# Optimization experiments

Measured on AMD Instinct MI355X. Metric: run time of the kernel, lower is better.

Reference implementation:

```python
import jax, jax.numpy as jnp
import numpy as np

HIDDEN = 512
STATE_DIM = 256
H = 8
D = STATE_DIM // H  # 32
B = 8
T = 4096


def setup_inputs() -> dict:
    key = jax.random.key(0)
    ks = jax.random.split(key, 12)
    s = 0.02
    return {
        "hidden_states": jax.random.normal(ks[0], (B, T, HIDDEN), jnp.float32),
        "state": jnp.zeros((B, H, D, D), jnp.float32),
        "W_k": jax.random.normal(ks[1], (STATE_DIM, HIDDEN), jnp.float32) * s,
        "W_v": jax.random.normal(ks[2], (STATE_DIM, HIDDEN), jnp.float32) * s,
        "W_q": jax.random.normal(ks[3], (STATE_DIM, HIDDEN), jnp.float32) * s,
        "W_beta": jax.random.normal(ks[4], (STATE_DIM, HIDDEN), jnp.float32) * s,
        "b_beta": jnp.zeros((STATE_DIM,), jnp.float32),
        "W_alpha": jax.random.normal(ks[5], (STATE_DIM, HIDDEN), jnp.float32) * s,
        "b_alpha": jnp.full((STATE_DIM,), 2.0, jnp.float32),
        "W_out": jax.random.normal(ks[6], (HIDDEN, STATE_DIM), jnp.float32) * s,
        "gate_W": jax.random.normal(ks[7], (STATE_DIM, HIDDEN), jnp.float32) * s,
        "norm_w": jnp.ones((STATE_DIM,), jnp.float32),
    }


def _rms_norm(x, w, eps=1e-6):
    dtype = x.dtype
    xf = x.astype(jnp.float32)
    n = xf * jax.lax.rsqrt(jnp.mean(xf * xf, axis=-1, keepdims=True) + eps)
    return (n * w).astype(dtype)


def reference(hidden_states, state, W_k, W_v, W_q, W_beta, b_beta, W_alpha, b_alpha, W_out, gate_W, norm_w):
    bsz, seq_len, _ = hidden_states.shape
    # projections -> (B, T, H, D)
    k = (hidden_states @ W_k.T).reshape(bsz, seq_len, H, D)
    v = (hidden_states @ W_v.T).reshape(bsz, seq_len, H, D)
    q = (hidden_states @ W_q.T).reshape(bsz, seq_len, H, D)
    beta = jax.nn.sigmoid(hidden_states @ W_beta.T + b_beta).reshape(bsz, seq_len, H, D)
    alpha = jax.nn.sigmoid(hidden_states @ W_alpha.T + b_alpha).reshape(bsz, seq_len, H, D)
    # F.normalize(k, dim=-1) with eps=1e-12
    k = k / jnp.maximum(jnp.linalg.norm(k, axis=-1, keepdims=True), 1e-12)
    gate = hidden_states @ gate_W.T  # (B, T, STATE_DIM)

    # time-major for scan: (T, B, H, D)
    def tm(x):
        return jnp.swapaxes(x, 0, 1)

    def step(S, inp):
        k_t, v_t, q_t, b_t, a_t = inp
        S = S * a_t[..., None]                              # row-wise decay
        pred = jnp.einsum('bhij,bhj->bhi', S, k_t)
        S = S + jnp.einsum('bhi,bhj->bhij', b_t * (v_t - pred), k_t)
        readout = jnp.einsum('bhij,bhj->bhi', S, q_t)       # (B, H, D)
        return S, readout

    S_final, readouts = jax.lax.scan(step, state, (tm(k), tm(v), tm(q), tm(beta), tm(alpha)))
    context = jnp.swapaxes(readouts, 0, 1).reshape(bsz, seq_len, STATE_DIM)
    context = _rms_norm(context, norm_w) * jax.nn.silu(gate)
    output = context @ W_out.T
    return output, S_final
```

## Files before the change

### kernel.cpp

```cpp
#include <hip/hip_runtime.h>
#include <stdint.h>

#define B_    8
#define T_    4096
#define HID   512
#define SD    256
#define NH    8
#define HD    32
#define M_TOK (B_*T_)
#define NPROJ 1536

typedef __attribute__((ext_vector_type(8))) short short8;
typedef __attribute__((ext_vector_type(4))) float f32x4;
typedef __attribute__((ext_vector_type(4))) float f4;
typedef __attribute__((ext_vector_type(2))) float f2;

__device__ __forceinline__ unsigned short f2bf(float f) {
  uint32_t u = __float_as_uint(f);
  uint32_t r = (u + 0x7fffu + ((u >> 16) & 1u)) >> 16;
  return (unsigned short)r;
}

__device__ __forceinline__ void gload16(const void* g, void* l) {
  __builtin_amdgcn_global_load_lds((const __attribute__((address_space(1))) void*)g,
                                   (__attribute__((address_space(3))) void*)l,
                                   16, 0, 0);
}

__device__ __forceinline__ float qred16(float x) {
  x += __int_as_float(__builtin_amdgcn_mov_dpp(__float_as_int(x), 0xB1,  0xF, 0xF, true));
  x += __int_as_float(__builtin_amdgcn_mov_dpp(__float_as_int(x), 0x4E,  0xF, 0xF, true));
  x += __int_as_float(__builtin_amdgcn_mov_dpp(__float_as_int(x), 0x141, 0xF, 0xF, true));
  x += __int_as_float(__builtin_amdgcn_mov_dpp(__float_as_int(x), 0x128, 0xF, 0xF, true));
  return x;
}

__device__ __forceinline__ float dpp_xor1(float x) {
  return __int_as_float(__builtin_amdgcn_mov_dpp(__float_as_int(x), 0xB1, 0xF, 0xF, true));
}

__global__ void cvt_f32_bf16(const float* __restrict__ in, unsigned short* __restrict__ out, int n4) {
  int i = blockIdx.x * blockDim.x + threadIdx.x;
  int stride = gridDim.x * blockDim.x;
  for (; i < n4; i += stride) {
    float4 v = reinterpret_cast<const float4*>(in)[i];
    ushort4 o;
    o.x = f2bf(v.x); o.y = f2bf(v.y); o.z = f2bf(v.z); o.w = f2bf(v.w);
    reinterpret_cast<ushort4*>(out)[i] = o;
  }
}

#define PM 128
#define PN 64
#define PK 64

__global__ void __launch_bounds__(256) proj_gemm(
    const unsigned short* __restrict__ hb, const unsigned short* __restrict__ Wc,
    const float* __restrict__ b_beta, const float* __restrict__ b_alpha,
    float* __restrict__ KQi, float* __restrict__ AVBf, float* __restrict__ gate)
{
  __shared__ unsigned short Asm[PM*PK];
  __shared__ unsigned short Bsm[3][PN*PK];
  const int t = threadIdx.x;
  const int w = t >> 6, lane = t & 63;
  const int bm0 = blockIdx.x * PM;
  const int role = blockIdx.y;
  const int grp = role >> 2;
  const int bn0 = (role & 3) * 64;
  const int pr0 = grp ? 4 : 0, pr1 = grp ? 1 : 2, pr2 = grp ? 3 : 5;

  f32x4 acc[3][2][4];
  #pragma unroll
  for (int pp = 0; pp < 3; ++pp)
    #pragma unroll
    for (int i = 0; i < 2; ++i)
      #pragma unroll
      for (int j = 0; j < 4; ++j) acc[pp][i][j] = (f32x4){0.f, 0.f, 0.f, 0.f};

  for (int k0 = 0; k0 < HID; k0 += PK) {
    #pragma unroll
    for (int it = 0; it < 4; ++it) {
      int unit = t + it * 256;
      int row = unit >> 3, seg = unit & 7;
      int dseg = seg ^ (row & 7);
      const unsigned short* g = hb + (size_t)(bm0 + row) * HID + k0 + dseg * 8;
      gload16(g, (char*)Asm + (w * 1024 + it * 4096));
    }
    #pragma unroll
    for (int pp = 0; pp < 3; ++pp) {
      const int pr = (pp == 0) ? pr0 : (pp == 1) ? pr1 : pr2;
      #pragma unroll
      for (int it = 0; it < 2; ++it) {
        int unit = t + it * 256;
        int n = unit >> 3, seg = unit & 7;
        int dseg = seg ^ (n & 7);
        const unsigned short* g = Wc + (size_t)(pr * 256 + bn0 + n) * HID + k0 + dseg * 8;
        gload16(g, (char*)Bsm[pp] + (w * 1024 + it * 4096));
      }
    }
    __syncthreads();
    #pragma unroll
    for (int ks = 0; ks < 2; ++ks) {
      short8 af[2];
      int u = ks * 4 + (lane >> 4);
      int slot = u ^ (lane & 7);
      #pragma unroll
      for (int rb = 0; rb < 2; ++rb) {
        int row = w * 32 + rb * 16 + (lane & 15);
        af[rb] = *(const short8*)((const char*)Asm + row * 128 + slot * 16);
      }
      #pragma unroll
      for (int pp = 0; pp < 3; ++pp) {
        short8 bfr[4];
        #pragma unroll
        for (int cb = 0; cb < 4; ++cb) {
          int nn = cb * 16 + (lane & 15);
          bfr[cb] = *(const short8*)((const char*)Bsm[pp] + nn * 128 + slot * 16);
        }
        #pragma unroll
        for (int rb = 0; rb < 2; ++rb)
          #pragma unroll
          for (int cb = 0; cb < 4; ++cb)
            acc[pp][rb][cb] = __builtin_amdgcn_mfma_f32_16x16x32_bf16(af[rb], bfr[cb], acc[pp][rb][cb], 0, 0, 0);
      }
    }
    __syncthreads();
  }

  if (grp == 0) {
    #pragma unroll
    for (int rb = 0; rb < 2; ++rb) {
      #pragma unroll
      for (int r = 0; r < 4; ++r) {
        float s0 = acc[0][rb][0][r] * acc[0][rb][0][r] + acc[0][rb][1][r] * acc[0][rb][1][r];
        float s1 = acc[0][rb][2][r] * acc[0][rb][2][r] + acc[0][rb][3][r] * acc[0][rb][3][r];
        s0 = qred16(s0); s1 = qred16(s1);
        float i0 = 1.0f / fmaxf(sqrtf(s0), 1e-12f);
        float i1 = 1.0f / fmaxf(sqrtf(s1), 1e-12f);
        acc[0][rb][0][r] *= i0; acc[0][rb][1][r] *= i0;
        acc[0][rb][2][r] *= i1; acc[0][rb][3][r] *= i1;
      }
    }
    #pragma unroll
    for (int rb = 0; rb < 2; ++rb) {
      #pragma unroll
      for (int cb = 0; cb < 4; ++cb) {
        int rem = bn0 + cb * 16 + (lane & 15);
        int h = rem >> 5, d = rem & 31;
        #pragma unroll
        for (int r = 0; r < 4; ++r) {
          int m = bm0 + w * 32 + rb * 16 + (lane >> 4) * 4 + r;
          int bb = m >> 12, tt = m & 4095;
          size_t tok = ((size_t)(bb * NH + h) * T_ + tt);
          float kv = acc[0][rb][cb][r], qv = acc[1][rb][cb][r];
          float kn = dpp_xor1(kv), qn = dpp_xor1(qv);
          if ((lane & 1) == 0)
            *(float4*)&KQi[tok * 64 + (d >> 1) * 4] = (float4){kv, kn, qv, qn};
          gate[(size_t)m * SD + rem] = acc[2][rb][cb][r];
        }
      }
    }
  } else {
    #pragma unroll
    for (int rb = 0; rb < 2; ++rb) {
      #pragma unroll
      for (int cb = 0; cb < 4; ++cb) {
        int rem = bn0 + cb * 16 + (lane & 15);
        int h = rem >> 5, d = rem & 31;
        #pragma unroll
        for (int r = 0; r < 4; ++r) {
          int m = bm0 + w * 32 + rb * 16 + (lane >> 4) * 4 + r;
          int bb = m >> 12, tt = m & 4095;
          size_t tok = ((size_t)(bb * NH + h) * T_ + tt);
          float av = 1.0f / (1.0f + expf(-(acc[0][rb][cb][r] + b_alpha[rem])));
          float vv = acc[1][rb][cb][r];
          float bv = 1.0f / (1.0f + expf(-(acc[2][rb][cb][r] + b_beta[rem])));
          *(float4*)&AVBf[(tok * HD + d) * 4] = (float4){av, vv, bv, 0.0f};
        }
      }
    }
  }
}

#define CH 32
#define NCH (T_/CH)

#define DSR(dst, areg, imm) \
  asm volatile("ds_read_b128 %0, %1 offset:%c2" : "=v"(dst) : "v"(areg), "i"(imm))

#define SHUF2(V,A,B) __builtin_shufflevector(V, V, A, B)

#define BAR asm volatile("s_barrier" ::: "memory")

__global__ void __launch_bounds__(128, 1) scan_kernel(
    const float* __restrict__ KQi, const float4* __restrict__ AVB,
    const float* __restrict__ state_in,
    float* __restrict__ ctx, float* __restrict__ Sfin)
{
  __shared__ __align__(16) char Lds[36864];
  const int blk = blockIdx.x;
  const int bh = blk & 63, rg = blk >> 6;
  const int b = bh >> 3, h = bh & 7;
  const int tid = threadIdx.x;
  const int wid = tid >> 6;
  const int lw = tid & 63;

  const float*  KQg = KQi + (size_t)bh * (T_ * 64);
  const float4* Vg  = AVB + (size_t)bh * (T_ * HD) + rg * 4;

  const uint32_t lds0 = (uint32_t)(uintptr_t)(__attribute__((address_space(3))) char*)&Lds[0];

  if (wid == 1) {
    const int il1 = lw >> 4, tq = lw & 15;
    const uint32_t a_pr = lds0 + 20480 + tq * 256 + il1 * 64;
    float* ctxb = ctx + (size_t)b * T_ * SD + h * HD + rg * 4 + il1;

    auto stageW = [&](int c2, int buf) {
      const float* kqg = KQg + (size_t)c2 * (CH * 64);
      #pragma unroll
      for (int it = 0; it < 8; ++it)
        gload16(kqg + (size_t)(lw + it * 64) * 4, Lds + buf * 8192 + it * 1024);
      const float4* vg = Vg + (size_t)c2 * (CH * HD);
      #pragma unroll
      for (int it = 0; it < 2; ++it) {
        int tc = it * 16 + (lw >> 2), r = lw & 3;
        gload16(vg + (size_t)tc * HD + r, Lds + 16384 + buf * 2048 + it * 1024);
      }
    };

#define REDUCE(PB, T0) do { \
      f4 r0_, r1_, r2_, r3_; \
      DSR(r0_, a_pr, (PB)*4096 + 0);  DSR(r1_, a_pr, (PB)*4096 + 16); \
      DSR(r2_, a_pr, (PB)*4096 + 32); DSR(r3_, a_pr, (PB)*4096 + 48); \
      asm volatile("s_waitcnt lgkmcnt(0)" : "+v"(r0_), "+v"(r1_), "+v"(r2_), "+v"(r3_)); \
      f4 s_ = (r0_ + r1_) + (r2_ + r3_); \
      float v_ = (s_.x + s_.y) + (s_.z + s_.w); \
      ctxb[(size_t)((T0) + tq) * SD] = v_; \
    } while (0)

    stageW(0, 0);
    asm volatile("s_waitcnt vmcnt(0)" ::: "memory");
    BAR;
    #pragma unroll 1
    for (int cp = 0; cp < NCH / 2; ++cp) {
      if (cp > 0) REDUCE(2, 64 * cp - 32);
      stageW(2 * cp + 1, 1);
      BAR;
      if (cp > 0) REDUCE(3, 64 * cp - 16);
      asm volatile("s_waitcnt vmcnt(0)" ::: "memory");
      BAR;
      REDUCE(0, 64 * cp);
      if (cp < NCH / 2 - 1) stageW(2 * cp + 2, 0);
      BAR;
      REDUCE(1, 64 * cp + 16);
      asm volatile("s_waitcnt vmcnt(0)" ::: "memory");
      BAR;
    }
    BAR;
    REDUCE(2, T_ - 32);
    REDUCE(3, T_ - 16);
#undef REDUCE
    return;
  }

  const int il = lw >> 4;
  const int p  = lw & 15;

  f2 S2;
  {
    const float* sp = state_in + (size_t)bh * 1024 + (rg * 4 + il) * 32 + p * 2;
    S2 = (f2){sp[0], sp[1]};
  }

  const uint32_t a_kq = lds0 + p * 16;
  const uint32_t a_v  = lds0 + 16384 + il * 16;
  const uint32_t a_pw = lds0 + 20480 + lw * 4;

#define C1(S, T, PB) do { \
    f2 k2_ = SHUF2(kq##S, 0, 1); \
    f2 q2_ = SHUF2(kq##S, 2, 3); \
    f4 VV_ = vv##S; \
    f2 as_ = (f2){VV_.x, VV_.x} * S2; \
    f2 d_  = k2_ * S2; \
    float pd_ = qred16(d_.x + d_.y); \
    float bv_ = VV_.y * VV_.z, ba_ = VV_.x * VV_.z; \
    float u_ = fmaf(-ba_, pd_, bv_); \
    S2 = __builtin_elementwise_fma((f2){u_, u_}, k2_, as_); \
    f2 o_ = q2_ * S2; \
    float po_ = o_.x + o_.y; \
    asm volatile("ds_write_b32 %0, %1 offset:%c2" :: "v"(a_pw), "v"(po_), "i"((PB)*4096 + ((T)&15)*256)); \
  } while (0)

  f4 kqA, vvA, kqB, vvB, kqC, vvC, kqD, vvD;

#define R1(S, BUF, T) do { \
    DSR(kq##S, a_kq, (BUF)*8192 + (T)*256); \
    DSR(vv##S, a_v,  (BUF)*2048 + (T)*64); \
  } while (0)

#define WKA(N, S) \
    asm volatile("s_waitcnt lgkmcnt(" #N ")" : "+v"(kq##S), "+v"(vv##S))

#define CHUNK(BUF, PBa, PBb) do { \
    R1(A,BUF,0); R1(B,BUF,1); R1(C,BUF,2); R1(D,BUF,3); \
    WKA(6,A); C1(A, 0,PBa); R1(A,BUF, 4); \
    WKA(7,B); C1(B, 1,PBa); R1(B,BUF, 5); \
    WKA(8,C); C1(C, 2,PBa); R1(C,BUF, 6); \
    WKA(9,D); C1(D, 3,PBa); R1(D,BUF, 7); \
    WKA(9,A); C1(A, 4,PBa); R1(A,BUF, 8); \
    WKA(9,B); C1(B, 5,PBa); R1(B,BUF, 9); \
    WKA(9,C); C1(C, 6,PBa); R1(C,BUF,10); \
    WKA(9,D); C1(D, 7,PBa); R1(D,BUF,11); \
    WKA(9,A); C1(A, 8,PBa); R1(A,BUF,12); \
    WKA(9,B); C1(B, 9,PBa); R1(B,BUF,13); \
    WKA(9,C); C1(C,10,PBa); R1(C,BUF,14); \
    WKA(9,D); C1(D,11,PBa); R1(D,BUF,15); \
    WKA(9,A); C1(A,12,PBa); R1(A,BUF,16); \
    WKA(9,B); C1(B,13,PBa); R1(B,BUF,17); \
    WKA(9,C); C1(C,14,PBa); R1(C,BUF,18); \
    WKA(9,D); C1(D,15,PBa); R1(D,BUF,19); \
    BAR; \
    WKA(9,A); C1(A,16,PBb); R1(A,BUF,20); \
    WKA(9,B); C1(B,17,PBb); R1(B,BUF,21); \
    WKA(9,C); C1(C,18,PBb); R1(C,BUF,22); \
    WKA(9,D); C1(D,19,PBb); R1(D,BUF,23); \
    WKA(9,A); C1(A,20,PBb); R1(A,BUF,24); \
    WKA(9,B); C1(B,21,PBb); R1(B,BUF,25); \
    WKA(9,C); C1(C,22,PBb); R1(C,BUF,26); \
    WKA(9,D); C1(D,23,PBb); R1(D,BUF,27); \
    WKA(9,A); C1(A,24,PBb); R1(A,BUF,28); \
    WKA(9,B); C1(B,25,PBb); R1(B,BUF,29); \
    WKA(9,C); C1(C,26,PBb); R1(C,BUF,30); \
    WKA(9,D); C1(D,27,PBb); R1(D,BUF,31); \
    WKA(9,A); C1(A,28,PBb); \
    WKA(7,B); C1(B,29,PBb); \
    WKA(5,C); C1(C,30,PBb); \
    WKA(3,D); C1(D,31,PBb); \
    BAR; \
  } while (0)

  BAR;
  #pragma unroll 1
  for (int cp = 0; cp < NCH / 2; ++cp) {
    CHUNK(0, 0, 1);
    CHUNK(1, 2, 3);
  }
  asm volatile("s_waitcnt lgkmcnt(0)" ::: "memory");
  BAR;

  {
    float* sp = Sfin + (size_t)bh * 1024 + (rg * 4 + il) * 32 + p * 2;
    sp[0] = S2.x; sp[1] = S2.y;
  }
#undef C1
#undef R1
#undef WKA
#undef CHUNK
}

__global__ void __launch_bounds__(256) rms_silu(
    const float* __restrict__ ctx, const float* __restrict__ gate,
    const float* __restrict__ norm_w, unsigned short* __restrict__ ctx2)
{
  size_t row = (size_t)blockIdx.x * 4 + (threadIdx.x >> 6);
  int lane = threadIdx.x & 63;
  const float4 x = *(const float4*)&ctx[row * SD + lane * 4];
  float s = x.x * x.x + x.y * x.y + x.z * x.z + x.w * x.w;
  #pragma unroll
  for (int m = 32; m >= 1; m >>= 1) s += __shfl_xor(s, m, 64);
  float rs = 1.0f / sqrtf(s * (1.0f / 256.0f) + 1e-6f);
  const float4 g = *(const float4*)&gate[row * SD + lane * 4];
  const float4 w = *(const float4*)&norm_w[lane * 4];
  ushort4 o;
  o.x = f2bf(x.x * rs * w.x * (g.x / (1.0f + expf(-g.x))));
  o.y = f2bf(x.y * rs * w.y * (g.y / (1.0f + expf(-g.y))));
  o.z = f2bf(x.z * rs * w.z * (g.z / (1.0f + expf(-g.z))));
  o.w = f2bf(x.w * rs * w.w * (g.w / (1.0f + expf(-g.w))));
  *(ushort4*)&ctx2[row * SD + lane * 4] = o;
}

__global__ void __launch_bounds__(256) out_gemm(
    const unsigned short* __restrict__ ctx2, const unsigned short* __restrict__ Wob,
    float* __restrict__ out)
{
  __shared__ unsigned short Asm[PM*PK];
  __shared__ unsigned short Bsm[PN*PK];
  const int t = threadIdx.x;
  const int w = t >> 6, lane = t & 63;
  const int bm0 = blockIdx.x * PM;
  const int bn0 = blockIdx.y * PN;

  f32x4 acc[2][4];
  #pragma unroll
  for (int i = 0; i < 2; ++i)
    #pragma unroll
    for (int j = 0; j < 4; ++j) acc[i][j] = (f32x4){0.f, 0.f, 0.f, 0.f};

  for (int k0 = 0; k0 < SD; k0 += PK) {
    #pragma unroll
    for (int it = 0; it < 4; ++it) {
      int unit = t + it * 256;
      int row = unit >> 3, seg = unit & 7;
      int dseg = seg ^ (row & 7);
      const unsigned short* g = ctx2 + (size_t)(bm0 + row) * SD + k0 + dseg * 8;
      gload16(g, (char*)Asm + (w * 1024 + it * 4096));
    }
    #pragma unroll
    for (int it = 0; it < 2; ++it) {
      int unit = t + it * 256;
      int n = unit >> 3, seg = unit & 7;
      int dseg = seg ^ (n & 7);
      const unsigned short* g = Wob + (size_t)(bn0 + n) * SD + k0 + dseg * 8;
      gload16(g, (char*)Bsm + (w * 1024 + it * 4096));
    }
    __syncthreads();
    #pragma unroll
    for (int ks = 0; ks < 2; ++ks) {
      short8 af[2], bfr[4];
      int u = ks * 4 + (lane >> 4);
      int slot = u ^ (lane & 7);
      #pragma unroll
      for (int rb = 0; rb < 2; ++rb) {
        int row = w * 32 + rb * 16 + (lane & 15);
        af[rb] = *(const short8*)((const char*)Asm + row * 128 + slot * 16);
      }
      #pragma unroll
      for (int cb = 0; cb < 4; ++cb) {
        int nn = cb * 16 + (lane & 15);
        bfr[cb] = *(const short8*)((const char*)Bsm + nn * 128 + slot * 16);
      }
      #pragma unroll
      for (int rb = 0; rb < 2; ++rb)
        #pragma unroll
        for (int cb = 0; cb < 4; ++cb)
          acc[rb][cb] = __builtin_amdgcn_mfma_f32_16x16x32_bf16(af[rb], bfr[cb], acc[rb][cb], 0, 0, 0);
    }
    __syncthreads();
  }
  #pragma unroll
  for (int rb = 0; rb < 2; ++rb)
    #pragma unroll
    for (int cb = 0; cb < 4; ++cb) {
      int n = bn0 + cb * 16 + (lane & 15);
      #pragma unroll
      for (int r = 0; r < 4; ++r) {
        int m = bm0 + w * 32 + rb * 16 + (lane >> 4) * 4 + r;
        out[(size_t)m * 512 + n] = acc[rb][cb][r];
      }
    }
}

extern "C" void kernel_launch(void* const* d_in, const int* in_sizes, int n_in,
                              void* d_out, int out_size, void* d_ws, size_t ws_size,
                              hipStream_t stream) {
  (void)in_sizes; (void)n_in; (void)out_size; (void)ws_size;
  const float* hidden  = (const float*)d_in[0];
  const float* state   = (const float*)d_in[1];
  const float* W_k     = (const float*)d_in[2];
  const float* W_v     = (const float*)d_in[3];
  const float* W_q     = (const float*)d_in[4];
  const float* W_beta  = (const float*)d_in[5];
  const float* b_beta  = (const float*)d_in[6];
  const float* W_alpha = (const float*)d_in[7];
  const float* b_alpha = (const float*)d_in[8];
  const float* W_out   = (const float*)d_in[9];
  const float* gate_W  = (const float*)d_in[10];
  const float* norm_w  = (const float*)d_in[11];
  float* out = (float*)d_out;

  char* ws = (char*)d_ws;
  unsigned short* hb  = (unsigned short*)(ws);
  unsigned short* Wc  = (unsigned short*)(ws + 33554432);
  unsigned short* Wob = (unsigned short*)(ws + 35127296);
  float* KQi  = (float*)(ws + 35389440);
  float* AVBf = (float*)(ws + 102498304);
  unsigned short* ctx2 = (unsigned short*)(ws + 236716032);
  float* ctx  = out;
  float* gate = out + 8388608;
  float* Sfin = out + 16777216;

  cvt_f32_bf16<<<2048, 256, 0, stream>>>(hidden, hb, M_TOK * HID / 4);
  cvt_f32_bf16<<<64, 256, 0, stream>>>(W_k,     Wc + 0 * 131072, 32768);
  cvt_f32_bf16<<<64, 256, 0, stream>>>(W_v,     Wc + 1 * 131072, 32768);
  cvt_f32_bf16<<<64, 256, 0, stream>>>(W_q,     Wc + 2 * 131072, 32768);
  cvt_f32_bf16<<<64, 256, 0, stream>>>(W_beta,  Wc + 3 * 131072, 32768);
  cvt_f32_bf16<<<64, 256, 0, stream>>>(W_alpha, Wc + 4 * 131072, 32768);
  cvt_f32_bf16<<<64, 256, 0, stream>>>(gate_W,  Wc + 5 * 131072, 32768);
  cvt_f32_bf16<<<64, 256, 0, stream>>>(W_out,   Wob, 32768);

  proj_gemm<<<dim3(256, 8), 256, 0, stream>>>(hb, Wc, b_beta, b_alpha, KQi, AVBf, gate);
  scan_kernel<<<512, 128, 0, stream>>>(KQi, (const float4*)AVBf, state, ctx, Sfin);
  rms_silu<<<8192, 256, 0, stream>>>(ctx, gate, norm_w, ctx2);
  out_gemm<<<dim3(256, 8), 256, 0, stream>>>(ctx2, Wob, out);
}
```

Measured before the change: 450.1 us.

## Give each scan lane four state columns and halve scan blocks

The scan kernel now has each lane own four state elements instead of two, so a block covers 8 state rows instead of 4. That halves the grid to 256 blocks and shortens the per-step cross-lane reduction to three DPP steps. The projection kernel changes the K/Q interleave layout to groups of four so each lane can read k and q with two 128-bit LDS reads. The LDS partial-sum ring is padded to a 272-byte stride to avoid bank conflicts. This trades parallelism (fewer blocks than CUs) for less shuffle latency and less redundant K/Q traffic per row, on a latency-bound serial scan.

After: 472.4 us. +5.0%, slower.

```diff
diff --git a/kernel.cpp b/kernel.cpp
--- a/kernel.cpp
+++ b/kernel.cpp
@@ -35,8 +35,21 @@
   return x;
 }
 
-__device__ __forceinline__ float dpp_xor1(float x) {
-  return __int_as_float(__builtin_amdgcn_mov_dpp(__float_as_int(x), 0xB1, 0xF, 0xF, true));
+__device__ __forceinline__ float qred8(float x) {
+  x += __int_as_float(__builtin_amdgcn_mov_dpp(__float_as_int(x), 0xB1,  0xF, 0xF, true));
+  x += __int_as_float(__builtin_amdgcn_mov_dpp(__float_as_int(x), 0x4E,  0xF, 0xF, true));
+  x += __int_as_float(__builtin_amdgcn_mov_dpp(__float_as_int(x), 0x141, 0xF, 0xF, true));
+  return x;
+}
+
+__device__ __forceinline__ float dpp_b1(float x) {
+  return __int_as_float(__builtin_amdgcn_mov_dpp(__float_as_int(x), 0x55, 0xF, 0xF, true));
+}
+__device__ __forceinline__ float dpp_b2(float x) {
+  return __int_as_float(__builtin_amdgcn_mov_dpp(__float_as_int(x), 0xAA, 0xF, 0xF, true));
+}
+__device__ __forceinline__ float dpp_b3(float x) {
+  return __int_as_float(__builtin_amdgcn_mov_dpp(__float_as_int(x), 0xFF, 0xF, 0xF, true));
 }
 
 __global__ void cvt_f32_bf16(const float* __restrict__ in, unsigned short* __restrict__ out, int n4) {
@@ -153,9 +166,13 @@
           int bb = m >> 12, tt = m & 4095;
           size_t tok = ((size_t)(bb * NH + h) * T_ + tt);
           float kv = acc[0][rb][cb][r], qv = acc[1][rb][cb][r];
-          float kn = dpp_xor1(kv), qn = dpp_xor1(qv);
-          if ((lane & 1) == 0)
-            *(float4*)&KQi[tok * 64 + (d >> 1) * 4] = (float4){kv, kn, qv, qn};
+          f4 kp = (f4){kv, dpp_b1(kv), dpp_b2(kv), dpp_b3(kv)};
+          f4 qp = (f4){qv, dpp_b1(qv), dpp_b2(qv), dpp_b3(qv)};
+          asm volatile("" : "+v"(kp), "+v"(qp));
+          if ((lane & 3) == 0) {
+            *(f4*)&KQi[tok * 64 + (d >> 2) * 8]     = kp;
+            *(f4*)&KQi[tok * 64 + (d >> 2) * 8 + 4] = qp;
+          }
           gate[(size_t)m * SD + rem] = acc[2][rb][cb][r];
         }
       }
@@ -184,6 +201,7 @@
 
 #define CH 32
 #define NCH (T_/CH)
+#define RING 24576
 
 #define DSR(dst, areg, imm) \
   asm volatile("ds_read_b128 %0, %1 offset:%c2" : "=v"(dst) : "v"(areg), "i"(imm))
@@ -197,7 +215,7 @@
     const float* __restrict__ state_in,
     float* __restrict__ ctx, float* __restrict__ Sfin)
 {
-  __shared__ __align__(16) char Lds[36864];
+  __shared__ __align__(16) char Lds[41984];
   const int blk = blockIdx.x;
   const int bh = blk & 63, rg = blk >> 6;
   const int b = bh >> 3, h = bh & 7;
@@ -206,14 +224,14 @@
   const int lw = tid & 63;
 
   const float*  KQg = KQi + (size_t)bh * (T_ * 64);
-  const float4* Vg  = AVB + (size_t)bh * (T_ * HD) + rg * 4;
+  const float4* Vg  = AVB + (size_t)bh * (T_ * HD) + rg * 8;
 
   const uint32_t lds0 = (uint32_t)(uintptr_t)(__attribute__((address_space(3))) char*)&Lds[0];
 
   if (wid == 1) {
-    const int il1 = lw >> 4, tq = lw & 15;
-    const uint32_t a_pr = lds0 + 20480 + tq * 256 + il1 * 64;
-    float* ctxb = ctx + (size_t)b * T_ * SD + h * HD + rg * 4 + il1;
+    const int il1 = lw >> 3, tq = lw & 7;
+    const uint32_t a_pr = lds0 + RING + tq * 272 + il1 * 32;
+    float* ctxb = ctx + (size_t)b * T_ * SD + h * HD + rg * 8 + il1;
 
     auto stageW = [&](int c2, int buf) {
       const float* kqg = KQg + (size_t)c2 * (CH * 64);
@@ -222,20 +240,22 @@
         gload16(kqg + (size_t)(lw + it * 64) * 4, Lds + buf * 8192 + it * 1024);
       const float4* vg = Vg + (size_t)c2 * (CH * HD);
       #pragma unroll
-      for (int it = 0; it < 2; ++it) {
-        int tc = it * 16 + (lw >> 2), r = lw & 3;
-        gload16(vg + (size_t)tc * HD + r, Lds + 16384 + buf * 2048 + it * 1024);
+      for (int it = 0; it < 4; ++it) {
+        int tt = it * 8 + (lw >> 3), rr = lw & 7;
+        gload16(vg + (size_t)tt * HD + rr, Lds + 16384 + buf * 4096 + it * 1024);
       }
     };
 
 #define REDUCE(PB, T0) do { \
       f4 r0_, r1_, r2_, r3_; \
-      DSR(r0_, a_pr, (PB)*4096 + 0);  DSR(r1_, a_pr, (PB)*4096 + 16); \
-      DSR(r2_, a_pr, (PB)*4096 + 32); DSR(r3_, a_pr, (PB)*4096 + 48); \
+      DSR(r0_, a_pr, (PB)*4352 + 0);    DSR(r1_, a_pr, (PB)*4352 + 16); \
+      DSR(r2_, a_pr, (PB)*4352 + 2176); DSR(r3_, a_pr, (PB)*4352 + 2192); \
       asm volatile("s_waitcnt lgkmcnt(0)" : "+v"(r0_), "+v"(r1_), "+v"(r2_), "+v"(r3_)); \
-      f4 s_ = (r0_ + r1_) + (r2_ + r3_); \
-      float v_ = (s_.x + s_.y) + (s_.z + s_.w); \
-      ctxb[(size_t)((T0) + tq) * SD] = v_; \
+      f4 sA_ = r0_ + r1_, sB_ = r2_ + r3_; \
+      float vA_ = (sA_.x + sA_.y) + (sA_.z + sA_.w); \
+      float vB_ = (sB_.x + sB_.y) + (sB_.z + sB_.w); \
+      ctxb[(size_t)((T0) + tq) * SD] = vA_; \
+      ctxb[(size_t)((T0) + tq + 8) * SD] = vB_; \
     } while (0)
 
     stageW(0, 0);
@@ -263,79 +283,84 @@
     return;
   }
 
-  const int il = lw >> 4;
-  const int p  = lw & 15;
-
-  f2 S2;
+  const int il = lw >> 3;
+  const int p  = lw & 7;
+
+  f2 S01, S23;
   {
-    const float* sp = state_in + (size_t)bh * 1024 + (rg * 4 + il) * 32 + p * 2;
-    S2 = (f2){sp[0], sp[1]};
-  }
-
-  const uint32_t a_kq = lds0 + p * 16;
+    const float* sp = state_in + (size_t)bh * 1024 + (rg * 8 + il) * 32 + p * 4;
+    float4 s0 = *(const float4*)sp;
+    S01 = (f2){s0.x, s0.y}; S23 = (f2){s0.z, s0.w};
+  }
+
+  const uint32_t a_kq = lds0 + p * 32;
   const uint32_t a_v  = lds0 + 16384 + il * 16;
-  const uint32_t a_pw = lds0 + 20480 + lw * 4;
+  const uint32_t a_pw = lds0 + RING + lw * 4;
 
 #define C1(S, T, PB) do { \
-    f2 k2_ = SHUF2(kq##S, 0, 1); \
-    f2 q2_ = SHUF2(kq##S, 2, 3); \
-    f4 VV_ = vv##S; \
-    f2 as_ = (f2){VV_.x, VV_.x} * S2; \
-    f2 d_  = k2_ * S2; \
-    float pd_ = qred16(d_.x + d_.y); \
+    f2 kl_ = SHUF2(k##S, 0, 1), kh_ = SHUF2(k##S, 2, 3); \
+    f2 ql_ = SHUF2(q##S, 0, 1), qh_ = SHUF2(q##S, 2, 3); \
+    f4 VV_ = v##S; \
+    f2 A2_ = (f2){VV_.x, VV_.x}; \
+    f2 as0_ = A2_ * S01, as1_ = A2_ * S23; \
+    f2 d_ = kl_ * S01; d_ = __builtin_elementwise_fma(kh_, S23, d_); \
+    float pd_ = qred8(d_.x + d_.y); \
     float bv_ = VV_.y * VV_.z, ba_ = VV_.x * VV_.z; \
     float u_ = fmaf(-ba_, pd_, bv_); \
-    S2 = __builtin_elementwise_fma((f2){u_, u_}, k2_, as_); \
-    f2 o_ = q2_ * S2; \
+    f2 U2_ = (f2){u_, u_}; \
+    S01 = __builtin_elementwise_fma(U2_, kl_, as0_); \
+    S23 = __builtin_elementwise_fma(U2_, kh_, as1_); \
+    f2 o_ = ql_ * S01; o_ = __builtin_elementwise_fma(qh_, S23, o_); \
     float po_ = o_.x + o_.y; \
-    asm volatile("ds_write_b32 %0, %1 offset:%c2" :: "v"(a_pw), "v"(po_), "i"((PB)*4096 + ((T)&15)*256)); \
+    asm volatile("ds_write_b32 %0, %1 offset:%c2" :: "v"(a_pw), "v"(po_), "i"((PB)*4352 + ((T)&15)*272)); \
   } while (0)
 
-  f4 kqA, vvA, kqB, vvB, kqC, vvC, kqD, vvD;
+  f4 kA, qA, vA, kB, qB, vB, kC, qC, vC, kD, qD, vD;
 
 #define R1(S, BUF, T) do { \
-    DSR(kq##S, a_kq, (BUF)*8192 + (T)*256); \
-    DSR(vv##S, a_v,  (BUF)*2048 + (T)*64); \
+    DSR(k##S, a_kq, (BUF)*8192 + (T)*256); \
+    DSR(q##S, a_kq, (BUF)*8192 + (T)*256 + 16); \
+    DSR(v##S, a_v,  (BUF)*4096 + (T)*128); \
   } while (0)
 
 #define WKA(N, S) \
-    asm volatile("s_waitcnt lgkmcnt(" #N ")" : "+v"(kq##S), "+v"(vv##S))
+    asm volatile("s_waitcnt lgkmcnt(" #N ")" : "+v"(k##S), "+v"(q##S), "+v"(v##S))
 
 #define CHUNK(BUF, PBa, PBb) do { \
     R1(A,BUF,0); R1(B,BUF,1); R1(C,BUF,2); R1(D,BUF,3); \
-    WKA(6,A); C1(A, 0,PBa); R1(A,BUF, 4); \
-    WKA(7,B); C1(B, 1,PBa); R1(B,BUF, 5); \
-    WKA(8,C); C1(C, 2,PBa); R1(C,BUF, 6); \
-    WKA(9,D); C1(D, 3,PBa); R1(D,BUF, 7); \
-    WKA(9,A); C1(A, 4,PBa); R1(A,BUF, 8); \
-    WKA(9,B); C1(B, 5,PBa); R1(B,BUF, 9); \
-    WKA(9,C); C1(C, 6,PBa); R1(C,BUF,10); \
-    WKA(9,D); C1(D, 7,PBa); R1(D,BUF,11); \
-    WKA(9,A); C1(A, 8,PBa); R1(A,BUF,12); \
-    WKA(9,B); C1(B, 9,PBa); R1(B,BUF,13); \
-    WKA(9,C); C1(C,10,PBa); R1(C,BUF,14); \
-    WKA(9,D); C1(D,11,PBa); R1(D,BUF,15); \
-    WKA(9,A); C1(A,12,PBa); R1(A,BUF,16); \
-    WKA(9,B); C1(B,13,PBa); R1(B,BUF,17); \
-    WKA(9,C); C1(C,14,PBa); R1(C,BUF,18); \
-    WKA(9,D); C1(D,15,PBa); R1(D,BUF,19); \
+    WKA(9 ,A); C1(A, 0,PBa); R1(A,BUF, 4); \
+    WKA(10,B); C1(B, 1,PBa); R1(B,BUF, 5); \
+    WKA(11,C); C1(C, 2,PBa); R1(C,BUF, 6); \
+    WKA(12,D); C1(D, 3,PBa); R1(D,BUF, 7); \
+    WKA(12,A); C1(A, 4,PBa); R1(A,BUF, 8); \
+    WKA(12,B); C1(B, 5,PBa); R1(B,BUF, 9); \
+    WKA(12,C); C1(C, 6,PBa); R1(C,BUF,10); \
+    WKA(12,D); C1(D, 7,PBa); R1(D,BUF,11); \
+    WKA(12,A); C1(A, 8,PBa); R1(A,BUF,12); \
+    WKA(12,B); C1(B, 9,PBa); R1(B,BUF,13); \
+    WKA(12,C); C1(C,10,PBa); R1(C,BUF,14); \
+    WKA(12,D); C1(D,11,PBa); R1(D,BUF,15); \
+    WKA(12,A); C1(A,12,PBa); R1(A,BUF,16); \
+    WKA(12,B); C1(B,13,PBa); R1(B,BUF,17); \
+    WKA(12,C); C1(C,14,PBa); R1(C,BUF,18); \
+    WKA(12,D); C1(D,15,PBa); R1(D,BUF,19); \
     BAR; \
-    WKA(9,A); C1(A,16,PBb); R1(A,BUF,20); \
-    WKA(9,B); C1(B,17,PBb); R1(B,BUF,21); \
-    WKA(9,C); C1(C,18,PBb); R1(C,BUF,22); \
-    WKA(9,D); C1(D,19,PBb); R1(D,BUF,23); \
-    WKA(9,A); C1(A,20,PBb); R1(A,BUF,24); \
-    WKA(9,B); C1(B,21,PBb); R1(B,BUF,25); \
-    WKA(9,C); C1(C,22,PBb); R1(C,BUF,26); \
-    WKA(9,D); C1(D,23,PBb); R1(D,BUF,27); \
-    WKA(9,A); C1(A,24,PBb); R1(A,BUF,28); \
-    WKA(9,B); C1(B,25,PBb); R1(B,BUF,29); \
-    WKA(9,C); C1(C,26,PBb); R1(C,BUF,30); \
-    WKA(9,D); C1(D,27,PBb); R1(D,BUF,31); \
-    WKA(9,A); C1(A,28,PBb); \
-    WKA(7,B); C1(B,29,PBb); \
-    WKA(5,C); C1(C,30,PBb); \
-    WKA(3,D); C1(D,31,PBb); \
+    WKA(12,A); C1(A,16,PBb); R1(A,BUF,20); \
+    WKA(12,B); C1(B,17,PBb); R1(B,BUF,21); \
+    WKA(12,C); C1(C,18,PBb); R1(C,BUF,22); \
+    WKA(12,D); C1(D,19,PBb); R1(D,BUF,23); \
+    WKA(12,A); C1(A,20,PBb); R1(A,BUF,24); \
+    WKA(12,B); C1(B,21,PBb); R1(B,BUF,25); \
+    WKA(12,C); C1(C,22,PBb); R1(C,BUF,26); \
+    WKA(12,D); C1(D,23,PBb); R1(D,BUF,27); \
+    WKA(12,A); C1(A,24,PBb); R1(A,BUF,28); \
+    WKA(12,B); C1(B,25,PBb); R1(B,BUF,29); \
+    WKA(12,C); C1(C,26,PBb); R1(C,BUF,30); \
+    WKA(12,D); C1(D,27,PBb); R1(D,BUF,31); \
+    WKA(12,A); C1(A,28,PBb); \
+    WKA(9 ,B); C1(B,29,PBb); \
+    WKA(6 ,C); C1(C,30,PBb); \
+    WKA(3 ,D); C1(D,31,PBb); \
     BAR; \
   } while (0)
 
@@ -349,8 +374,8 @@
   BAR;
 
   {
-    float* sp = Sfin + (size_t)bh * 1024 + (rg * 4 + il) * 32 + p * 2;
-    sp[0] = S2.x; sp[1] = S2.y;
+    float* sp = Sfin + (size_t)bh * 1024 + (rg * 8 + il) * 32 + p * 4;
+    *(float4*)sp = (float4){S01.x, S01.y, S23.x, S23.y};
   }
 #undef C1
 #undef R1
@@ -489,7 +514,7 @@
   cvt_f32_bf16<<<64, 256, 0, stream>>>(W_out,   Wob, 32768);
 
   proj_gemm<<<dim3(256, 8), 256, 0, stream>>>(hb, Wc, b_beta, b_alpha, KQi, AVBf, gate);
-  scan_kernel<<<512, 128, 0, stream>>>(KQi, (const float4*)AVBf, state, ctx, Sfin);
+  scan_kernel<<<256, 128, 0, stream>>>(KQi, (const float4*)AVBf, state, ctx, Sfin);
   rms_silu<<<8192, 256, 0, stream>>>(ctx, gate, norm_w, ctx2);
   out_gemm<<<dim3(256, 8), 256, 0, stream>>>(ctx2, Wob, out);
 }
```

## Process two timesteps per scan step using precomputed k·k overlap; merge weight conversions

Applied to the files above, without the earlier changes.

The scan's inner step now advances the recurrence two timesteps at a time. It uses the dot product of consecutive keys (k_t·k_{t+1}), which the helper wave computes from global memory and writes into the V LDS slot. Both predictions are then taken from the same state, so the two cross-lane reductions can overlap instead of being serialized. Separately, the seven weight conversion launches are merged into one 2D-grid kernel. This adds extra global loads and a blocking LDS write per chunk in the helper wave, and relies on an unused V slot being available.

Measured after the change: 432.4 us. 3.9% less time.

```diff
diff --git a/kernel.cpp b/kernel.cpp
--- a/kernel.cpp
+++ b/kernel.cpp
@@ -8,7 +8,6 @@
 #define NH    8
 #define HD    32
 #define M_TOK (B_*T_)
-#define NPROJ 1536
 
 typedef __attribute__((ext_vector_type(8))) short short8;
 typedef __attribute__((ext_vector_type(4))) float f32x4;
@@ -48,6 +47,24 @@
     o.x = f2bf(v.x); o.y = f2bf(v.y); o.z = f2bf(v.z); o.w = f2bf(v.w);
     reinterpret_cast<ushort4*>(out)[i] = o;
   }
+}
+
+__global__ void __launch_bounds__(256) cvt_weights(
+    const float* __restrict__ W_k, const float* __restrict__ W_v,
+    const float* __restrict__ W_q, const float* __restrict__ W_beta,
+    const float* __restrict__ W_alpha, const float* __restrict__ gate_W,
+    const float* __restrict__ W_out,
+    unsigned short* __restrict__ Wc, unsigned short* __restrict__ Wob)
+{
+  int slice = blockIdx.y;
+  const float* src = (slice == 0) ? W_k : (slice == 1) ? W_v : (slice == 2) ? W_q :
+                     (slice == 3) ? W_beta : (slice == 4) ? W_alpha : (slice == 5) ? gate_W : W_out;
+  unsigned short* dst = (slice == 6) ? Wob : (Wc + slice * 131072);
+  int i = blockIdx.x * 256 + threadIdx.x;
+  float4 v = reinterpret_cast<const float4*>(src)[i];
+  ushort4 o;
+  o.x = f2bf(v.x); o.y = f2bf(v.y); o.z = f2bf(v.z); o.w = f2bf(v.w);
+  reinterpret_cast<ushort4*>(dst)[i] = o;
 }
 
 #define PM 128
@@ -215,6 +232,10 @@
     const uint32_t a_pr = lds0 + 20480 + tq * 256 + il1 * 64;
     float* ctxb = ctx + (size_t)b * T_ * SD + h * HD + rg * 4 + il1;
 
+    const int gpp = lw >> 2, gqt = lw & 3;
+    f4 gx0, gx1, gx2, gx3, gy0, gy1, gy2, gy3;
+    const uint32_t a_gw = lds0 + 16384 + (2 * gpp) * 64 + gqt * 16 + 12;
+
     auto stageW = [&](int c2, int buf) {
       const float* kqg = KQg + (size_t)c2 * (CH * 64);
       #pragma unroll
@@ -226,6 +247,27 @@
         int tc = it * 16 + (lw >> 2), r = lw & 3;
         gload16(vg + (size_t)tc * HD + r, Lds + 16384 + buf * 2048 + it * 1024);
       }
+    };
+
+    auto gfetch = [&](int c2) {
+      const float* gp = KQg + ((size_t)c2 * CH + 2 * gpp) * 64 + gqt * 16;
+      gx0 = *(const f4*)(gp);      gx1 = *(const f4*)(gp + 4);
+      gx2 = *(const f4*)(gp + 8);  gx3 = *(const f4*)(gp + 12);
+      gy0 = *(const f4*)(gp + 64); gy1 = *(const f4*)(gp + 68);
+      gy2 = *(const f4*)(gp + 72); gy3 = *(const f4*)(gp + 76);
+    };
+
+    auto gwrite = [&](int buf) {
+      f2 g2 = SHUF2(gx0, 0, 1) * SHUF2(gy0, 0, 1);
+      g2 = __builtin_elementwise_fma(SHUF2(gx1, 0, 1), SHUF2(gy1, 0, 1), g2);
+      g2 = __builtin_elementwise_fma(SHUF2(gx2, 0, 1), SHUF2(gy2, 0, 1), g2);
+      g2 = __builtin_elementwise_fma(SHUF2(gx3, 0, 1), SHUF2(gy3, 0, 1), g2);
+      float G = g2.x + g2.y;
+      G += __int_as_float(__builtin_amdgcn_mov_dpp(__float_as_int(G), 0xB1, 0xF, 0xF, true));
+      G += __int_as_float(__builtin_amdgcn_mov_dpp(__float_as_int(G), 0x4E, 0xF, 0xF, true));
+      uint32_t aw = a_gw + buf * 2048;
+      asm volatile("ds_write_b32 %0, %1" :: "v"(aw), "v"(G));
+      asm volatile("s_waitcnt lgkmcnt(0)" ::: "memory");
     };
 
 #define REDUCE(PB, T0) do { \
@@ -238,22 +280,27 @@
       ctxb[(size_t)((T0) + tq) * SD] = v_; \
     } while (0)
 
+    gfetch(0);
     stageW(0, 0);
     asm volatile("s_waitcnt vmcnt(0)" ::: "memory");
+    gwrite(0);
     BAR;
     #pragma unroll 1
     for (int cp = 0; cp < NCH / 2; ++cp) {
       if (cp > 0) REDUCE(2, 64 * cp - 32);
+      gfetch(2 * cp + 1);
       stageW(2 * cp + 1, 1);
       BAR;
       if (cp > 0) REDUCE(3, 64 * cp - 16);
       asm volatile("s_waitcnt vmcnt(0)" ::: "memory");
+      gwrite(1);
       BAR;
       REDUCE(0, 64 * cp);
-      if (cp < NCH / 2 - 1) stageW(2 * cp + 2, 0);
+      if (cp < NCH / 2 - 1) { gfetch(2 * cp + 2); stageW(2 * cp + 2, 0); }
       BAR;
       REDUCE(1, 64 * cp + 16);
       asm volatile("s_waitcnt vmcnt(0)" ::: "memory");
+      if (cp < NCH / 2 - 1) gwrite(0);
       BAR;
     }
     BAR;
@@ -276,66 +323,61 @@
   const uint32_t a_v  = lds0 + 16384 + il * 16;
   const uint32_t a_pw = lds0 + 20480 + lw * 4;
 
-#define C1(S, T, PB) do { \
-    f2 k2_ = SHUF2(kq##S, 0, 1); \
-    f2 q2_ = SHUF2(kq##S, 2, 3); \
-    f4 VV_ = vv##S; \
-    f2 as_ = (f2){VV_.x, VV_.x} * S2; \
-    f2 d_  = k2_ * S2; \
-    float pd_ = qred16(d_.x + d_.y); \
-    float bv_ = VV_.y * VV_.z, ba_ = VV_.x * VV_.z; \
-    float u_ = fmaf(-ba_, pd_, bv_); \
-    S2 = __builtin_elementwise_fma((f2){u_, u_}, k2_, as_); \
-    f2 o_ = q2_ * S2; \
-    float po_ = o_.x + o_.y; \
-    asm volatile("ds_write_b32 %0, %1 offset:%c2" :: "v"(a_pw), "v"(po_), "i"((PB)*4096 + ((T)&15)*256)); \
+  f4 kqA, vvA, kqB, vvB, kqC, vvC, kqD, vvD;
+
+#define R2(X, Y, BUF, J) do { \
+    DSR(kq##X, a_kq, (BUF)*8192 + (2*(J))*256); \
+    DSR(vv##X, a_v,  (BUF)*2048 + (2*(J))*64); \
+    DSR(kq##Y, a_kq, (BUF)*8192 + (2*(J)+1)*256); \
+    DSR(vv##Y, a_v,  (BUF)*2048 + (2*(J)+1)*64); \
   } while (0)
 
-  f4 kqA, vvA, kqB, vvB, kqC, vvC, kqD, vvD;
-
-#define R1(S, BUF, T) do { \
-    DSR(kq##S, a_kq, (BUF)*8192 + (T)*256); \
-    DSR(vv##S, a_v,  (BUF)*2048 + (T)*64); \
+#define WKA2(N, X, Y) \
+    asm volatile("s_waitcnt lgkmcnt(" #N ")" \
+                 : "+v"(kq##X), "+v"(vv##X), "+v"(kq##Y), "+v"(vv##Y))
+
+#define C2(X, Y, T0, PB) do { \
+    f2 k0_ = SHUF2(kq##X, 0, 1), q0_ = SHUF2(kq##X, 2, 3); \
+    f2 k1_ = SHUF2(kq##Y, 0, 1), q1_ = SHUF2(kq##Y, 2, 3); \
+    f4 VA_ = vv##X, VB_ = vv##Y; \
+    f2 dA_ = k0_ * S2, dB_ = k1_ * S2; \
+    float W0_ = qred16(dA_.x + dA_.y); \
+    float W1_ = qred16(dB_.x + dB_.y); \
+    float u0_ = fmaf(-(VA_.z * VA_.x), W0_, VA_.z * VA_.y); \
+    float bua_ = VB_.z * VB_.x; \
+    float c2_ = bua_ * VA_.w; \
+    float c1_ = fmaf(-(bua_ * VA_.x), W1_, VB_.z * VB_.y); \
+    float u1_ = fmaf(-c2_, u0_, c1_); \
+    f2 St_ = __builtin_elementwise_fma((f2){u0_, u0_}, k0_, (f2){VA_.x, VA_.x} * S2); \
+    f2 Su_ = __builtin_elementwise_fma((f2){u1_, u1_}, k1_, (f2){VB_.x, VB_.x} * St_); \
+    f2 o0_ = q0_ * St_; \
+    f2 o1_ = q1_ * Su_; \
+    float p0_ = o0_.x + o0_.y; \
+    float p1_ = o1_.x + o1_.y; \
+    S2 = Su_; \
+    asm volatile("ds_write_b32 %0, %1 offset:%c2" :: "v"(a_pw), "v"(p0_), "i"((PB)*4096 + ((T0)&15)*256)); \
+    asm volatile("ds_write_b32 %0, %1 offset:%c2" :: "v"(a_pw), "v"(p1_), "i"((PB)*4096 + (((T0)+1)&15)*256)); \
   } while (0)
 
-#define WKA(N, S) \
-    asm volatile("s_waitcnt lgkmcnt(" #N ")" : "+v"(kq##S), "+v"(vv##S))
-
 #define CHUNK(BUF, PBa, PBb) do { \
-    R1(A,BUF,0); R1(B,BUF,1); R1(C,BUF,2); R1(D,BUF,3); \
-    WKA(6,A); C1(A, 0,PBa); R1(A,BUF, 4); \
-    WKA(7,B); C1(B, 1,PBa); R1(B,BUF, 5); \
-    WKA(8,C); C1(C, 2,PBa); R1(C,BUF, 6); \
-    WKA(9,D); C1(D, 3,PBa); R1(D,BUF, 7); \
-    WKA(9,A); C1(A, 4,PBa); R1(A,BUF, 8); \
-    WKA(9,B); C1(B, 5,PBa); R1(B,BUF, 9); \
-    WKA(9,C); C1(C, 6,PBa); R1(C,BUF,10); \
-    WKA(9,D); C1(D, 7,PBa); R1(D,BUF,11); \
-    WKA(9,A); C1(A, 8,PBa); R1(A,BUF,12); \
-    WKA(9,B); C1(B, 9,PBa); R1(B,BUF,13); \
-    WKA(9,C); C1(C,10,PBa); R1(C,BUF,14); \
-    WKA(9,D); C1(D,11,PBa); R1(D,BUF,15); \
-    WKA(9,A); C1(A,12,PBa); R1(A,BUF,16); \
-    WKA(9,B); C1(B,13,PBa); R1(B,BUF,17); \
-    WKA(9,C); C1(C,14,PBa); R1(C,BUF,18); \
-    WKA(9,D); C1(D,15,PBa); R1(D,BUF,19); \
+    R2(A,B,BUF,0); R2(C,D,BUF,1); \
+    WKA2(4,A,B); C2(A,B, 0,PBa); R2(A,B,BUF,2); \
+    WKA2(6,C,D); C2(C,D, 2,PBa); R2(C,D,BUF,3); \
+    WKA2(6,A,B); C2(A,B, 4,PBa); R2(A,B,BUF,4); \
+    WKA2(6,C,D); C2(C,D, 6,PBa); R2(C,D,BUF,5); \
+    WKA2(6,A,B); C2(A,B, 8,PBa); R2(A,B,BUF,6); \
+    WKA2(6,C,D); C2(C,D,10,PBa); R2(C,D,BUF,7); \
+    WKA2(6,A,B); C2(A,B,12,PBa); R2(A,B,BUF,8); \
+    WKA2(6,C,D); C2(C,D,14,PBa); R2(C,D,BUF,9); \
     BAR; \
-    WKA(9,A); C1(A,16,PBb); R1(A,BUF,20); \
-    WKA(9,B); C1(B,17,PBb); R1(B,BUF,21); \
-    WKA(9,C); C1(C,18,PBb); R1(C,BUF,22); \
-    WKA(9,D); C1(D,19,PBb); R1(D,BUF,23); \
-    WKA(9,A); C1(A,20,PBb); R1(A,BUF,24); \
-    WKA(9,B); C1(B,21,PBb); R1(B,BUF,25); \
-    WKA(9,C); C1(C,22,PBb); R1(C,BUF,26); \
-    WKA(9,D); C1(D,23,PBb); R1(D,BUF,27); \
-    WKA(9,A); C1(A,24,PBb); R1(A,BUF,28); \
-    WKA(9,B); C1(B,25,PBb); R1(B,BUF,29); \
-    WKA(9,C); C1(C,26,PBb); R1(C,BUF,30); \
-    WKA(9,D); C1(D,27,PBb); R1(D,BUF,31); \
-    WKA(9,A); C1(A,28,PBb); \
-    WKA(7,B); C1(B,29,PBb); \
-    WKA(5,C); C1(C,30,PBb); \
-    WKA(3,D); C1(D,31,PBb); \
+    WKA2(6,A,B); C2(A,B,16,PBb); R2(A,B,BUF,10); \
+    WKA2(6,C,D); C2(C,D,18,PBb); R2(C,D,BUF,11); \
+    WKA2(6,A,B); C2(A,B,20,PBb); R2(A,B,BUF,12); \
+    WKA2(6,C,D); C2(C,D,22,PBb); R2(C,D,BUF,13); \
+    WKA2(6,A,B); C2(A,B,24,PBb); R2(A,B,BUF,14); \
+    WKA2(6,C,D); C2(C,D,26,PBb); R2(C,D,BUF,15); \
+    WKA2(6,A,B); C2(A,B,28,PBb); \
+    WKA2(2,C,D); C2(C,D,30,PBb); \
     BAR; \
   } while (0)
 
@@ -352,9 +394,9 @@
     float* sp = Sfin + (size_t)bh * 1024 + (rg * 4 + il) * 32 + p * 2;
     sp[0] = S2.x; sp[1] = S2.y;
   }
-#undef C1
-#undef R1
-#undef WKA
+#undef C2
+#undef R2
+#undef WKA2
 #undef CHUNK
 }
 
@@ -480,13 +522,7 @@
   float* Sfin = out + 16777216;
 
   cvt_f32_bf16<<<2048, 256, 0, stream>>>(hidden, hb, M_TOK * HID / 4);
-  cvt_f32_bf16<<<64, 256, 0, stream>>>(W_k,     Wc + 0 * 131072, 32768);
-  cvt_f32_bf16<<<64, 256, 0, stream>>>(W_v,     Wc + 1 * 131072, 32768);
-  cvt_f32_bf16<<<64, 256, 0, stream>>>(W_q,     Wc + 2 * 131072, 32768);
-  cvt_f32_bf16<<<64, 256, 0, stream>>>(W_beta,  Wc + 3 * 131072, 32768);
-  cvt_f32_bf16<<<64, 256, 0, stream>>>(W_alpha, Wc + 4 * 131072, 32768);
-  cvt_f32_bf16<<<64, 256, 0, stream>>>(gate_W,  Wc + 5 * 131072, 32768);
-  cvt_f32_bf16<<<64, 256, 0, stream>>>(W_out,   Wob, 32768);
+  cvt_weights<<<dim3(128, 7), 256, 0, stream>>>(W_k, W_v, W_q, W_beta, W_alpha, gate_W, W_out, Wc, Wob);
 
   proj_gemm<<<dim3(256, 8), 256, 0, stream>>>(hb, Wc, b_beta, b_alpha, KQi, AVBf, gate);
   scan_kernel<<<512, 128, 0, stream>>>(KQi, (const float4*)AVBf, state, ctx, Sfin);
```
